# Optimization experiments

Hardware: AMD Instinct MI355X
Metric: run time of the kernel (lower is better)

Reference implementation:

```python
import jax, jax.numpy as jnp
import numpy as np

B, SQ, SKV, DIN, DOUT = 8, 2048, 2048, 512, 512

def setup_inputs() -> dict:
    key = jax.random.key(0)
    ks = jax.random.split(key, 8)
    s = 1.0 / np.sqrt(DIN)
    return {
        "query": jax.random.normal(ks[0], (B, SQ, DIN), jnp.float32),
        "key": jax.random.normal(ks[1], (B, SKV, DIN), jnp.float32),
        "value": jax.random.normal(ks[2], (B, SKV, DIN), jnp.float32),
        "offset": jax.random.normal(ks[3], (B, SQ, DIN), jnp.float32),
        "Wq": jax.random.normal(ks[4], (DIN, DOUT), jnp.float32) * s,
        "Wk": jax.random.normal(ks[5], (DIN, DOUT), jnp.float32) * s,
        "Wv": jax.random.normal(ks[6], (DIN, DOUT), jnp.float32) * s,
        "Woff": jax.random.normal(ks[7], (DIN, SKV), jnp.float32) * s,
    }

def reference(query, key, value, offset, Wq, Wk, Wv, Woff):
    # q/k/v projections (nn.Linear, no bias)
    q = jnp.einsum("bqi,io->bqo", query, Wq)   # [B,SQ,DOUT]
    k = jnp.einsum("bki,io->bko", key, Wk)     # [B,SKV,DOUT]
    v = jnp.einsum("bki,io->bko", value, Wv)   # [B,SKV,DOUT]
    scale = 1.0 / jnp.sqrt(jnp.asarray(q.shape[-1], jnp.float32))
    scores = jnp.einsum("bqd,bkd->bqk", q, k) * scale  # [B,SQ,SKV]
    attn = jax.nn.softmax(scores, axis=-1)
    # offset bias is added AFTER softmax (no renormalization), per original
    attn = attn + jnp.einsum("bqi,ik->bqk", offset, Woff)
    return jnp.einsum("bqk,bkd->bqd", attn, v)  # [B,SQ,DOUT]
```

## Files before the change

### kernel.cpp

```cpp
#include <hip/hip_runtime.h>
#include <hip/hip_bf16.h>
#include <stdint.h>

typedef __bf16 bf16;
typedef bf16 bf16x4_t __attribute__((ext_vector_type(4)));
typedef bf16 bf16x8_t __attribute__((ext_vector_type(8)));
typedef float floatx4_t __attribute__((ext_vector_type(4)));

#define NB 8
#define SQ 2048
#define SKV 2048
#define DIN 512
#define DOUT 512

__device__ __forceinline__ void load_lds16(const bf16* g, bf16* l) {
    __builtin_amdgcn_global_load_lds(
        (const __attribute__((address_space(1))) unsigned int*)g,
        (__attribute__((address_space(3))) unsigned int*)l, 16, 0, 0);
}

struct CastArgs {
    const float* src[6];
    bf16* dst[6];
    int n4[6];
};
__global__ void cast_many(CastArgs a) {
    int z = blockIdx.z;
    int i = blockIdx.x * blockDim.x + threadIdx.x;
    if (i >= a.n4[z]) return;
    if (!a.src[z]) {
        bf16x4_t zo = { (bf16)0.f, (bf16)0.f, (bf16)0.f, (bf16)0.f };
        ((bf16x4_t*)a.dst[z])[i] = zo;
        return;
    }
    float4 f = ((const float4*)a.src[z])[i];
    bf16x4_t o = { (bf16)f.x, (bf16)f.y, (bf16)f.z, (bf16)f.w };
    ((bf16x4_t*)a.dst[z])[i] = o;
}

struct TWArgs { const float* src[3]; bf16* dst[3]; float scl[3]; };
__global__ void transpose_w(TWArgs a) {
    __shared__ float t[32][33];
    const float* src = a.src[blockIdx.z];
    bf16* dst = a.dst[blockIdx.z];
    const float s = a.scl[blockIdx.z];
    int tx = threadIdx.x, ty = threadIdx.y;
    int x0 = blockIdx.x * 32, y0 = blockIdx.y * 32;
#pragma unroll
    for (int j = 0; j < 4; ++j)
        t[ty + 8 * j][tx] = src[(y0 + ty + 8 * j) * DIN + x0 + tx];
    __syncthreads();
#pragma unroll
    for (int j = 0; j < 4; ++j)
        dst[(x0 + ty + 8 * j) * DIN + y0 + tx] = (bf16)(t[tx][ty + 8 * j] * s);
}

__global__ void transpose_v(const bf16* Vb, bf16* VT) {
    __shared__ bf16 t[32][33];
    const bf16* src = Vb + (long long)blockIdx.z * SKV * DOUT;
    bf16* dst = VT + (long long)blockIdx.z * DOUT * SKV;
    int tx = threadIdx.x, ty = threadIdx.y;
    int x0 = blockIdx.x * 32, y0 = blockIdx.y * 32;
#pragma unroll
    for (int j = 0; j < 4; ++j)
        t[ty + 8 * j][tx] = src[(long long)(y0 + ty + 8 * j) * DOUT + x0 + tx];
    __syncthreads();
#pragma unroll
    for (int j = 0; j < 4; ++j)
        dst[(long long)(x0 + ty + 8 * j) * SKV + y0 + tx] = t[tx][ty + 8 * j];
}

__device__ __forceinline__ void gemm_mainloop(
    floatx4_t (&acc)[4][4], const bf16* __restrict__ Ap, const bf16* __restrict__ Bp,
    int lda, int ldb, int K, bf16* As, bf16* Bs, int wave, int lane)
{
    const int wm = (wave & 1) * 64, wn = (wave >> 1) * 64;
    const int lm = lane & 15, quad = lane >> 4;
    const int srow = lane >> 2, scol = (lane & 3) * 8;
    for (int k0 = 0; k0 < K; k0 += 32) {
        __syncthreads();
#pragma unroll
        for (int t = 0; t < 2; ++t) {
            const int r0 = (wave * 2 + t) * 16;
            load_lds16(Ap + (long long)(r0 + srow) * lda + (k0 + scol), &As[r0 * 32]);
            load_lds16(Bp + (long long)(r0 + srow) * ldb + (k0 + scol), &Bs[r0 * 32]);
        }
        __syncthreads();
        bf16x8_t af[4], bfr[4];
#pragma unroll
        for (int i = 0; i < 4; ++i)
            af[i] = *(const bf16x8_t*)&As[(wm + i * 16 + lm) * 32 + quad * 8];
#pragma unroll
        for (int i = 0; i < 4; ++i)
            bfr[i] = *(const bf16x8_t*)&Bs[(wn + i * 16 + lm) * 32 + quad * 8];
#pragma unroll
        for (int i = 0; i < 4; ++i)
#pragma unroll
            for (int j = 0; j < 4; ++j)
                acc[i][j] = __builtin_amdgcn_mfma_f32_16x16x32_bf16(af[i], bfr[j], acc[i][j], 0, 0, 0);
    }
}

__global__ __launch_bounds__(256) void proj_gemm(
    const bf16* __restrict__ A0, const bf16* __restrict__ B0, bf16* __restrict__ C0)
{
    __shared__ bf16 As[128 * 32];
    __shared__ bf16 Bs[128 * 32];
    const int tid = threadIdx.x;
    const int wave = tid >> 6, lane = tid & 63;
    const int id = blockIdx.x;
    const int xcd = id & 7, t = id >> 3, m = t & 3;
    const int gg = xcd + 8 * (t >> 2);
    const int y = gg & 127, z = gg >> 7;

    floatx4_t acc[4][4];
#pragma unroll
    for (int i = 0; i < 4; ++i)
#pragma unroll
        for (int j = 0; j < 4; ++j) acc[i][j] = 0.0f;

    const bf16* Ap = A0 + (long long)z * (NB * SQ * DIN) + (long long)y * 128 * DIN;
    const bf16* Bp = B0 + (long long)z * (DIN * DOUT) + (long long)m * 128 * DIN;
    gemm_mainloop(acc, Ap, Bp, DIN, DIN, DIN, As, Bs, wave, lane);

    const int wm = (wave & 1) * 64, wn = (wave >> 1) * 64;
    const int lm = lane & 15, quad = lane >> 4;
    bf16* C = C0 + (long long)z * (NB * SQ * DOUT);
#pragma unroll
    for (int i = 0; i < 4; ++i)
#pragma unroll
        for (int j = 0; j < 4; ++j) {
            const long long row0 = (long long)y * 128 + wm + i * 16 + quad * 4;
            const int col = m * 128 + wn + j * 16 + lm;
#pragma unroll
            for (int r = 0; r < 4; ++r)
                C[(row0 + r) * DOUT + col] = (bf16)acc[i][j][r];
        }
}

__global__ __launch_bounds__(256) void g_gemm(
    const bf16* __restrict__ VT, const bf16* __restrict__ Woffb, bf16* __restrict__ G)
{
    __shared__ bf16 As[128 * 32];
    __shared__ bf16 Bs[128 * 32];
    const int tid = threadIdx.x;
    const int wave = tid >> 6, lane = tid & 63;
    const int id = blockIdx.x;
    const int z = id & 7, x = (id >> 3) & 3, y = (id >> 3) >> 2;

    floatx4_t acc[4][4];
#pragma unroll
    for (int i = 0; i < 4; ++i)
#pragma unroll
        for (int j = 0; j < 4; ++j) acc[i][j] = 0.0f;

    const bf16* Ap = VT + (long long)z * (DOUT * SKV) + (long long)y * 128 * SKV;
    const bf16* Bp = Woffb + (long long)x * 128 * SKV;
    gemm_mainloop(acc, Ap, Bp, SKV, SKV, SKV, As, Bs, wave, lane);

    const int wm = (wave & 1) * 64, wn = (wave >> 1) * 64;
    const int lm = lane & 15, quad = lane >> 4;
    bf16* C = G + (long long)z * (DOUT * DIN);
#pragma unroll
    for (int i = 0; i < 4; ++i)
#pragma unroll
        for (int j = 0; j < 4; ++j) {
            const long long row0 = (long long)y * 128 + wm + i * 16 + quad * 4;
            const int col = x * 128 + wn + j * 16 + lm;
#pragma unroll
            for (int r = 0; r < 4; ++r)
                C[(row0 + r) * DIN + col] = (bf16)acc[i][j][r];
        }
}

__global__ __launch_bounds__(256) void s_gemm_exp(
    const bf16* __restrict__ Qb, const bf16* __restrict__ Kb,
    bf16* __restrict__ expS, float* __restrict__ l)
{
    __shared__ bf16 As[128 * 32];
    __shared__ bf16 Bs[128 * 32];
    const int tid = threadIdx.x;
    const int wave = tid >> 6, lane = tid & 63;
    const int id = blockIdx.x;
    const int z = id & 7, x = (id >> 3) & 15, y = (id >> 3) >> 4;

    floatx4_t acc[4][4];
#pragma unroll
    for (int i = 0; i < 4; ++i)
#pragma unroll
        for (int j = 0; j < 4; ++j) acc[i][j] = 0.0f;

    const bf16* Ap = Qb + ((long long)z * SQ + (long long)y * 128) * DOUT;
    const bf16* Bp = Kb + ((long long)z * SKV + (long long)x * 128) * DOUT;
    gemm_mainloop(acc, Ap, Bp, DOUT, DOUT, DOUT, As, Bs, wave, lane);

    const int wm = (wave & 1) * 64, wn = (wave >> 1) * 64;
    const int lm = lane & 15, quad = lane >> 4;
    bf16* C = expS + (long long)z * SQ * SKV;
    const long long grow0 = (long long)z * SQ + (long long)y * 128;
#pragma unroll
    for (int i = 0; i < 4; ++i) {
        float rs[4] = {0.f, 0.f, 0.f, 0.f};
#pragma unroll
        for (int j = 0; j < 4; ++j) {
            const long long row0 = (long long)y * 128 + wm + i * 16 + quad * 4;
            const int col = x * 128 + wn + j * 16 + lm;
#pragma unroll
            for (int r = 0; r < 4; ++r) {
                float e = __expf(acc[i][j][r]);
                rs[r] += e;
                C[(row0 + r) * SKV + col] = (bf16)e;
            }
        }
#pragma unroll
        for (int r = 0; r < 4; ++r) {
            float v = rs[r];
            v += __shfl_xor(v, 1, 64);
            v += __shfl_xor(v, 2, 64);
            v += __shfl_xor(v, 4, 64);
            v += __shfl_xor(v, 8, 64);
            if (lm == 0)
                atomicAdd(&l[grow0 + wm + i * 16 + quad * 4 + r], v);
        }
    }
}

__global__ __launch_bounds__(256) void out_gemm(
    const bf16* __restrict__ expS, const bf16* __restrict__ VT,
    const bf16* __restrict__ offb, const bf16* __restrict__ G,
    const float* __restrict__ l, float* __restrict__ out)
{
    __shared__ bf16 As[128 * 32];
    __shared__ bf16 Bs[128 * 32];
    const int tid = threadIdx.x;
    const int wave = tid >> 6, lane = tid & 63;
    const int id = blockIdx.x;
    const int z = id & 7, x = (id >> 3) & 3, y = (id >> 3) >> 2;

    floatx4_t acc[4][4];
#pragma unroll
    for (int i = 0; i < 4; ++i)
#pragma unroll
        for (int j = 0; j < 4; ++j) acc[i][j] = 0.0f;

    {
        const bf16* Ap = expS + (long long)z * SQ * SKV + (long long)y * 128 * SKV;
        const bf16* Bp = VT + (long long)z * DOUT * SKV + (long long)x * 128 * SKV;
        gemm_mainloop(acc, Ap, Bp, SKV, SKV, SKV, As, Bs, wave, lane);
    }

    const int wm = (wave & 1) * 64, wn = (wave >> 1) * 64;
    const int lm = lane & 15, quad = lane >> 4;
    const long long grow0 = (long long)z * SQ + (long long)y * 128;

#pragma unroll
    for (int i = 0; i < 4; ++i)
#pragma unroll
        for (int r = 0; r < 4; ++r) {
            const float inv = 1.0f / l[grow0 + wm + i * 16 + quad * 4 + r];
#pragma unroll
            for (int j = 0; j < 4; ++j) acc[i][j][r] *= inv;
        }

    {
        const bf16* Ap = offb + (grow0) * DIN;
        const bf16* Bp = G + (long long)z * DOUT * DIN + (long long)x * 128 * DIN;
        gemm_mainloop(acc, Ap, Bp, DIN, DIN, DIN, As, Bs, wave, lane);
    }

#pragma unroll
    for (int i = 0; i < 4; ++i)
#pragma unroll
        for (int j = 0; j < 4; ++j) {
            const long long row0 = grow0 + wm + i * 16 + quad * 4;
            const int col = x * 128 + wn + j * 16 + lm;
#pragma unroll
            for (int r = 0; r < 4; ++r)
                out[(row0 + r) * DOUT + col] = acc[i][j][r];
        }
}

extern "C" void kernel_launch(void* const* d_in, const int* in_sizes, int n_in,
                              void* d_out, int out_size, void* d_ws, size_t ws_size,
                              hipStream_t stream) {
    const float* query = (const float*)d_in[0];
    const float* key_ = (const float*)d_in[1];
    const float* value = (const float*)d_in[2];
    const float* offset = (const float*)d_in[3];
    const float* Wq = (const float*)d_in[4];
    const float* Wk = (const float*)d_in[5];
    const float* Wv = (const float*)d_in[6];
    const float* Woff = (const float*)d_in[7];
    float* out = (float*)d_out;

    char* ws = (char*)d_ws;
    const long long NE = (long long)NB * SQ * DIN;

    const long long MB = 1048576;
    bf16* queryb  = (bf16*)(ws + 0 * MB);
    bf16* keyb    = (bf16*)(ws + 16 * MB);
    bf16* valueb  = (bf16*)(ws + 32 * MB);
    bf16* offsetb = (bf16*)(ws + 48 * MB);
    bf16* Qb      = (bf16*)(ws + 64 * MB);
    bf16* Kb      = (bf16*)(ws + 80 * MB);
    bf16* Vb      = (bf16*)(ws + 96 * MB);
    bf16* VT      = (bf16*)(ws + 112 * MB);
    bf16* G       = (bf16*)(ws + 128 * MB);
    bf16* WqT     = (bf16*)(ws + 132 * MB);
    bf16* WkT     = (bf16*)(ws + 132 * MB + 524288);
    bf16* WvT     = (bf16*)(ws + 132 * MB + 1048576);
    bf16* Woffb   = (bf16*)(ws + 132 * MB + 1572864);
    float* lbuf   = (float*)(ws + 136 * MB);
    bf16* expS    = (bf16*)(ws + 137 * MB);

    CastArgs ca;
    ca.src[0] = query;  ca.dst[0] = queryb;  ca.n4[0] = (int)(NE / 4);
    ca.src[1] = key_;   ca.dst[1] = keyb;    ca.n4[1] = (int)(NE / 4);
    ca.src[2] = value;  ca.dst[2] = valueb;  ca.n4[2] = (int)(NE / 4);
    ca.src[3] = offset; ca.dst[3] = offsetb; ca.n4[3] = (int)(NE / 4);
    ca.src[4] = Woff;   ca.dst[4] = Woffb;   ca.n4[4] = (DIN * SKV) / 4;
    ca.src[5] = nullptr; ca.dst[5] = (bf16*)lbuf; ca.n4[5] = (NB * SQ * 4) / 8;
    cast_many<<<dim3(8192, 1, 6), 256, 0, stream>>>(ca);

    TWArgs tw;
    tw.src[0] = Wq; tw.src[1] = Wk; tw.src[2] = Wv;
    tw.dst[0] = WqT; tw.dst[1] = WkT; tw.dst[2] = WvT;
    tw.scl[0] = 0.04419417382415922f; tw.scl[1] = 1.0f; tw.scl[2] = 1.0f;
    transpose_w<<<dim3(16, 16, 3), dim3(32, 8), 0, stream>>>(tw);

    proj_gemm<<<dim3(1536), 256, 0, stream>>>(queryb, WqT, Qb);

    transpose_v<<<dim3(DOUT / 32, SKV / 32, NB), dim3(32, 8), 0, stream>>>(Vb, VT);

    g_gemm<<<dim3(128), 256, 0, stream>>>(VT, Woffb, G);

    s_gemm_exp<<<dim3(2048), 256, 0, stream>>>(Qb, Kb, expS, lbuf);

    out_gemm<<<dim3(512), 256, 0, stream>>>(expS, VT, offsetb, G, lbuf, out);
}
```

Measured before the change: 375.4 us.

## Compute V projection directly transposed and double the GEMM K-step to 64

The V projection is now computed as WvT × valueᵀ inside the projection kernel, so it writes VT directly and the separate transpose_v kernel and the Vb buffer go away. The shared GEMM mainloop now stages two 32-wide K slices per iteration, which halves the number of barrier pairs at the cost of doubling LDS per block. The projection launch now has 1024 Q/K blocks plus 512 V blocks. The larger LDS footprint may reduce the number of blocks resident per CU.

```diff
diff --git a/kernel.cpp b/kernel.cpp
--- a/kernel.cpp
+++ b/kernel.cpp
@@ -55,21 +55,6 @@
         dst[(x0 + ty + 8 * j) * DIN + y0 + tx] = (bf16)(t[tx][ty + 8 * j] * s);
 }
 
-__global__ void transpose_v(const bf16* Vb, bf16* VT) {
-    __shared__ bf16 t[32][33];
-    const bf16* src = Vb + (long long)blockIdx.z * SKV * DOUT;
-    bf16* dst = VT + (long long)blockIdx.z * DOUT * SKV;
-    int tx = threadIdx.x, ty = threadIdx.y;
-    int x0 = blockIdx.x * 32, y0 = blockIdx.y * 32;
-#pragma unroll
-    for (int j = 0; j < 4; ++j)
-        t[ty + 8 * j][tx] = src[(long long)(y0 + ty + 8 * j) * DOUT + x0 + tx];
-    __syncthreads();
-#pragma unroll
-    for (int j = 0; j < 4; ++j)
-        dst[(long long)(x0 + ty + 8 * j) * SKV + y0 + tx] = t[tx][ty + 8 * j];
-}
-
 __device__ __forceinline__ void gemm_mainloop(
     floatx4_t (&acc)[4][4], const bf16* __restrict__ Ap, const bf16* __restrict__ Bp,
     int lda, int ldb, int K, bf16* As, bf16* Bs, int wave, int lane)
@@ -77,41 +62,49 @@
     const int wm = (wave & 1) * 64, wn = (wave >> 1) * 64;
     const int lm = lane & 15, quad = lane >> 4;
     const int srow = lane >> 2, scol = (lane & 3) * 8;
-    for (int k0 = 0; k0 < K; k0 += 32) {
+    for (int k0 = 0; k0 < K; k0 += 64) {
         __syncthreads();
 #pragma unroll
-        for (int t = 0; t < 2; ++t) {
-            const int r0 = (wave * 2 + t) * 16;
-            load_lds16(Ap + (long long)(r0 + srow) * lda + (k0 + scol), &As[r0 * 32]);
-            load_lds16(Bp + (long long)(r0 + srow) * ldb + (k0 + scol), &Bs[r0 * 32]);
+        for (int p = 0; p < 2; ++p) {
+#pragma unroll
+            for (int t = 0; t < 2; ++t) {
+                const int r0 = (wave * 2 + t) * 16;
+                load_lds16(Ap + (long long)(r0 + srow) * lda + (k0 + p * 32 + scol),
+                           &As[p * 4096 + r0 * 32]);
+                load_lds16(Bp + (long long)(r0 + srow) * ldb + (k0 + p * 32 + scol),
+                           &Bs[p * 4096 + r0 * 32]);
+            }
         }
         __syncthreads();
-        bf16x8_t af[4], bfr[4];
-#pragma unroll
-        for (int i = 0; i < 4; ++i)
-            af[i] = *(const bf16x8_t*)&As[(wm + i * 16 + lm) * 32 + quad * 8];
-#pragma unroll
-        for (int i = 0; i < 4; ++i)
-            bfr[i] = *(const bf16x8_t*)&Bs[(wn + i * 16 + lm) * 32 + quad * 8];
-#pragma unroll
-        for (int i = 0; i < 4; ++i)
-#pragma unroll
-            for (int j = 0; j < 4; ++j)
-                acc[i][j] = __builtin_amdgcn_mfma_f32_16x16x32_bf16(af[i], bfr[j], acc[i][j], 0, 0, 0);
+#pragma unroll
+        for (int p = 0; p < 2; ++p) {
+            bf16x8_t af[4], bfr[4];
+#pragma unroll
+            for (int i = 0; i < 4; ++i)
+                af[i] = *(const bf16x8_t*)&As[p * 4096 + (wm + i * 16 + lm) * 32 + quad * 8];
+#pragma unroll
+            for (int i = 0; i < 4; ++i)
+                bfr[i] = *(const bf16x8_t*)&Bs[p * 4096 + (wn + i * 16 + lm) * 32 + quad * 8];
+#pragma unroll
+            for (int i = 0; i < 4; ++i)
+#pragma unroll
+                for (int j = 0; j < 4; ++j)
+                    acc[i][j] = __builtin_amdgcn_mfma_f32_16x16x32_bf16(af[i], bfr[j], acc[i][j], 0, 0, 0);
+        }
     }
 }
 
 __global__ __launch_bounds__(256) void proj_gemm(
-    const bf16* __restrict__ A0, const bf16* __restrict__ B0, bf16* __restrict__ C0)
-{
-    __shared__ bf16 As[128 * 32];
-    __shared__ bf16 Bs[128 * 32];
+    const bf16* __restrict__ QKin, const bf16* __restrict__ WqkT, bf16* __restrict__ QKout,
+    const bf16* __restrict__ valueb, const bf16* __restrict__ WvT, bf16* __restrict__ VT)
+{
+    __shared__ bf16 As[2 * 128 * 32];
+    __shared__ bf16 Bs[2 * 128 * 32];
     const int tid = threadIdx.x;
     const int wave = tid >> 6, lane = tid & 63;
+    const int wm = (wave & 1) * 64, wn = (wave >> 1) * 64;
+    const int lm = lane & 15, quad = lane >> 4;
     const int id = blockIdx.x;
-    const int xcd = id & 7, t = id >> 3, m = t & 3;
-    const int gg = xcd + 8 * (t >> 2);
-    const int y = gg & 127, z = gg >> 7;
 
     floatx4_t acc[4][4];
 #pragma unroll
@@ -119,30 +112,50 @@
 #pragma unroll
         for (int j = 0; j < 4; ++j) acc[i][j] = 0.0f;
 
-    const bf16* Ap = A0 + (long long)z * (NB * SQ * DIN) + (long long)y * 128 * DIN;
-    const bf16* Bp = B0 + (long long)z * (DIN * DOUT) + (long long)m * 128 * DIN;
-    gemm_mainloop(acc, Ap, Bp, DIN, DIN, DIN, As, Bs, wave, lane);
-
-    const int wm = (wave & 1) * 64, wn = (wave >> 1) * 64;
-    const int lm = lane & 15, quad = lane >> 4;
-    bf16* C = C0 + (long long)z * (NB * SQ * DOUT);
-#pragma unroll
-    for (int i = 0; i < 4; ++i)
-#pragma unroll
-        for (int j = 0; j < 4; ++j) {
-            const long long row0 = (long long)y * 128 + wm + i * 16 + quad * 4;
-            const int col = m * 128 + wn + j * 16 + lm;
-#pragma unroll
-            for (int r = 0; r < 4; ++r)
-                C[(row0 + r) * DOUT + col] = (bf16)acc[i][j][r];
-        }
+    if (id < 1024) {
+        const int xcd = id & 7, t = id >> 3, m = t & 3;
+        const int gg = xcd + 8 * (t >> 2);
+        const int y = gg & 127, z = gg >> 7;
+        const bf16* Ap = QKin + (long long)z * (NB * SQ * DIN) + (long long)y * 128 * DIN;
+        const bf16* Bp = WqkT + (long long)z * (DIN * DOUT) + (long long)m * 128 * DIN;
+        gemm_mainloop(acc, Ap, Bp, DIN, DIN, DIN, As, Bs, wave, lane);
+        bf16* C = QKout + (long long)z * (NB * SQ * DOUT);
+#pragma unroll
+        for (int i = 0; i < 4; ++i)
+#pragma unroll
+            for (int j = 0; j < 4; ++j) {
+                const long long row0 = (long long)y * 128 + wm + i * 16 + quad * 4;
+                const int col = m * 128 + wn + j * 16 + lm;
+#pragma unroll
+                for (int r = 0; r < 4; ++r)
+                    C[(row0 + r) * DOUT + col] = (bf16)acc[i][j][r];
+            }
+    } else {
+        const int id2 = id - 1024;
+        const int z = id2 & 7, r2 = id2 >> 3;
+        const int ym = r2 & 3, xn = r2 >> 2;
+        const bf16* Ap = WvT + (long long)ym * 128 * DIN;
+        const bf16* Bp = valueb + (long long)z * (SKV * DIN) + (long long)xn * 128 * DIN;
+        gemm_mainloop(acc, Ap, Bp, DIN, DIN, DIN, As, Bs, wave, lane);
+        bf16* C = VT + (long long)z * (DOUT * SKV);
+#pragma unroll
+        for (int i = 0; i < 4; ++i)
+#pragma unroll
+            for (int j = 0; j < 4; ++j) {
+                const long long row0 = (long long)ym * 128 + wm + i * 16 + quad * 4;
+                const int col = xn * 128 + wn + j * 16 + lm;
+#pragma unroll
+                for (int r = 0; r < 4; ++r)
+                    C[(row0 + r) * SKV + col] = (bf16)acc[i][j][r];
+            }
+    }
 }
 
 __global__ __launch_bounds__(256) void g_gemm(
     const bf16* __restrict__ VT, const bf16* __restrict__ Woffb, bf16* __restrict__ G)
 {
-    __shared__ bf16 As[128 * 32];
-    __shared__ bf16 Bs[128 * 32];
+    __shared__ bf16 As[2 * 128 * 32];
+    __shared__ bf16 Bs[2 * 128 * 32];
     const int tid = threadIdx.x;
     const int wave = tid >> 6, lane = tid & 63;
     const int id = blockIdx.x;
@@ -177,8 +190,8 @@
     const bf16* __restrict__ Qb, const bf16* __restrict__ Kb,
     bf16* __restrict__ expS, float* __restrict__ l)
 {
-    __shared__ bf16 As[128 * 32];
-    __shared__ bf16 Bs[128 * 32];
+    __shared__ bf16 As[2 * 128 * 32];
+    __shared__ bf16 Bs[2 * 128 * 32];
     const int tid = threadIdx.x;
     const int wave = tid >> 6, lane = tid & 63;
     const int id = blockIdx.x;
@@ -230,8 +243,8 @@
     const bf16* __restrict__ offb, const bf16* __restrict__ G,
     const float* __restrict__ l, float* __restrict__ out)
 {
-    __shared__ bf16 As[128 * 32];
-    __shared__ bf16 Bs[128 * 32];
+    __shared__ bf16 As[2 * 128 * 32];
+    __shared__ bf16 Bs[2 * 128 * 32];
     const int tid = threadIdx.x;
     const int wave = tid >> 6, lane = tid & 63;
     const int id = blockIdx.x;
@@ -303,15 +316,14 @@
     bf16* offsetb = (bf16*)(ws + 48 * MB);
     bf16* Qb      = (bf16*)(ws + 64 * MB);
     bf16* Kb      = (bf16*)(ws + 80 * MB);
-    bf16* Vb      = (bf16*)(ws + 96 * MB);
-    bf16* VT      = (bf16*)(ws + 112 * MB);
-    bf16* G       = (bf16*)(ws + 128 * MB);
-    bf16* WqT     = (bf16*)(ws + 132 * MB);
-    bf16* WkT     = (bf16*)(ws + 132 * MB + 524288);
-    bf16* WvT     = (bf16*)(ws + 132 * MB + 1048576);
-    bf16* Woffb   = (bf16*)(ws + 132 * MB + 1572864);
-    float* lbuf   = (float*)(ws + 136 * MB);
-    bf16* expS    = (bf16*)(ws + 137 * MB);
+    bf16* VT      = (bf16*)(ws + 96 * MB);
+    bf16* G       = (bf16*)(ws + 112 * MB);
+    bf16* WqT     = (bf16*)(ws + 116 * MB);
+    bf16* WkT     = (bf16*)(ws + 116 * MB + 524288);
+    bf16* WvT     = (bf16*)(ws + 116 * MB + 1048576);
+    bf16* Woffb   = (bf16*)(ws + 116 * MB + 1572864);
+    float* lbuf   = (float*)(ws + 120 * MB);
+    bf16* expS    = (bf16*)(ws + 121 * MB);
 
     CastArgs ca;
     ca.src[0] = query;  ca.dst[0] = queryb;  ca.n4[0] = (int)(NE / 4);
@@ -328,9 +340,7 @@
     tw.scl[0] = 0.04419417382415922f; tw.scl[1] = 1.0f; tw.scl[2] = 1.0f;
     transpose_w<<<dim3(16, 16, 3), dim3(32, 8), 0, stream>>>(tw);
 
-    proj_gemm<<<dim3(1536), 256, 0, stream>>>(queryb, WqT, Qb);
-
-    transpose_v<<<dim3(DOUT / 32, SKV / 32, NB), dim3(32, 8), 0, stream>>>(Vb, VT);
+    proj_gemm<<<dim3(1536), 256, 0, stream>>>(queryb, WqT, Qb, valueb, WvT, VT);
 
     g_gemm<<<dim3(128), 256, 0, stream>>>(VT, Woffb, G);
 
```

After: 374.8 us. No clear change (-0.2%).
